# Kernel optimization log

Measured on AMD Instinct MI355X. Metric: run time of the kernel, lower is better.

The kernel has to match this reference:

```python
import jax, jax.numpy as jnp
import numpy as np

NUM_HEADS = 8
NUM_GROUPS = 32
EPS = 1e-5


def setup_inputs() -> dict:
    key = jax.random.key(0)
    ks = jax.random.split(key, 12)
    B, C, H, W = 8, 512, 32, 32
    E = 512
    s = 1.0 / np.sqrt(C)
    inp = {
        "input_tensor": jax.random.normal(ks[0], (B, C, H, W), dtype=jnp.float32),
        "Wq": jax.random.normal(ks[1], (C, E), dtype=jnp.float32) * s,
        "bq": jnp.zeros((E,), dtype=jnp.float32),
        "Wk": jax.random.normal(ks[2], (C, E), dtype=jnp.float32) * s,
        "bk": jnp.zeros((E,), dtype=jnp.float32),
        "Wv": jax.random.normal(ks[3], (C, E), dtype=jnp.float32) * s,
        "bv": jnp.zeros((E,), dtype=jnp.float32),
        "Wo": jax.random.normal(ks[4], (E, E), dtype=jnp.float32) * s,
        "bo": jnp.zeros((E,), dtype=jnp.float32),
        "gamma": jnp.ones((E,), dtype=jnp.float32),
        "beta": jnp.zeros((E,), dtype=jnp.float32),
    }
    return inp


def reference(input_tensor, Wq, bq, Wk, bk, Wv, bv, Wo, bo, gamma, beta):
    B, C, H, W = input_tensor.shape
    E = Wq.shape[1]
    nH = NUM_HEADS
    hd = E // nH
    S = H * W

    # [B, C, H, W] -> [B, S, C]
    x = input_tensor.reshape(B, C, S).transpose(0, 2, 1)

    q = (x @ Wq + bq).reshape(B, S, nH, hd).transpose(0, 2, 1, 3)  # [B, h, S, d]
    k = (x @ Wk + bk).reshape(B, S, nH, hd).transpose(0, 2, 1, 3)
    v = (x @ Wv + bv).reshape(B, S, nH, hd).transpose(0, 2, 1, 3)

    scale = hd ** (-0.5)
    scores = jnp.einsum("bhqd,bhkd->bhqk", q, k) * scale
    weights = jax.nn.softmax(scores, axis=-1)
    attn = jnp.einsum("bhqk,bhkd->bhqd", weights, v)  # [B, h, S, d]

    attn = attn.transpose(0, 2, 1, 3).reshape(B, S, E)
    out = attn @ Wo + bo  # [B, S, E]
    out = out.transpose(0, 2, 1).reshape(B, E, H, W)

    y = out + input_tensor

    # GroupNorm over (channels_per_group, H, W)
    G = NUM_GROUPS
    yg = y.reshape(B, G, E // G, H, W)
    mean = jnp.mean(yg, axis=(2, 3, 4), keepdims=True)
    var = jnp.var(yg, axis=(2, 3, 4), keepdims=True)
    yn = ((yg - mean) * jax.lax.rsqrt(var + EPS)).reshape(B, E, H, W)
    return yn * gamma[None, :, None, None] + beta[None, :, None, None]
```

## Files before the change

kernel.cpp:

```cpp
#include <hip/hip_runtime.h>
#include <math.h>

constexpr int Bn  = 8;
constexpr int Cc  = 512;
constexpr int Ss  = 1024;
constexpr int Ee  = 512;
constexpr int nHd = 8;
constexpr int Hd  = 64;
constexpr int Gg  = 32;
constexpr int Cpg = 16;

typedef __bf16 bf16x8 __attribute__((ext_vector_type(8)));
typedef float  f32x4  __attribute__((ext_vector_type(4)));
typedef float  f32x16 __attribute__((ext_vector_type(16)));

__device__ inline __bf16 cvt_bf16(float f) {
    unsigned u = __builtin_bit_cast(unsigned, f);
    u += 0x7fffu + ((u >> 16) & 1u);
    unsigned short h = (unsigned short)(u >> 16);
    return __builtin_bit_cast(__bf16, h);
}

__device__ inline void gld16(const __bf16* g, __bf16* l) {
    __builtin_amdgcn_global_load_lds(
        (const __attribute__((address_space(1))) void*)g,
        (__attribute__((address_space(3))) void*)l, 16, 0, 0);
}

__device__ inline unsigned pk_bf16_rtz(float hi, float lo) {
    return __builtin_amdgcn_perm(__builtin_bit_cast(unsigned, hi),
                                 __builtin_bit_cast(unsigned, lo), 0x07060302u);
}

__global__ __launch_bounds__(256) void transpose_x(
    const float* __restrict__ x, __bf16* __restrict__ xt)
{
    const int b = blockIdx.z, c0 = blockIdx.y * 32, s0 = blockIdx.x * 32;
    __shared__ float T[32][33];
    const int r8 = threadIdx.x >> 5, c32 = threadIdx.x & 31;
#pragma unroll
    for (int i = 0; i < 4; i++)
        T[r8 + i * 8][c32] = x[((size_t)b * Cc + c0 + r8 + i * 8) * Ss + s0 + c32];
    __syncthreads();
#pragma unroll
    for (int i = 0; i < 4; i++)
        xt[((size_t)b * Ss + s0 + r8 + i * 8) * Cc + c0 + c32] =
            cvt_bf16(T[c32][r8 + i * 8]);
}

__global__ __launch_bounds__(256) void transpose_w(
    const float* __restrict__ w0, const float* __restrict__ w1,
    const float* __restrict__ w2, const float* __restrict__ w3,
    __bf16* __restrict__ d0, __bf16* __restrict__ d1,
    __bf16* __restrict__ d2, __bf16* __restrict__ d3)
{
    const int m = blockIdx.z;
    const float* src = (m == 0) ? w0 : (m == 1) ? w1 : (m == 2) ? w2 : w3;
    __bf16* dst = (m == 0) ? d0 : (m == 1) ? d1 : (m == 2) ? d2 : d3;
    const int e0 = blockIdx.x * 32, c0 = blockIdx.y * 32;
    __shared__ float T[32][33];
    const int r8 = threadIdx.x >> 5, c32 = threadIdx.x & 31;
#pragma unroll
    for (int i = 0; i < 4; i++)
        T[r8 + i * 8][c32] = src[(size_t)(c0 + r8 + i * 8) * Ee + e0 + c32];
    __syncthreads();
#pragma unroll
    for (int i = 0; i < 4; i++)
        dst[(size_t)(e0 + r8 + i * 8) * Cc + c0 + c32] = cvt_bf16(T[c32][r8 + i * 8]);
}

__global__ __launch_bounds__(256) void qkv_mfma(
    const __bf16* __restrict__ xt,
    const __bf16* __restrict__ wqt, const __bf16* __restrict__ wkt,
    const __bf16* __restrict__ wvt,
    const float* __restrict__ bq, const float* __restrict__ bk,
    const float* __restrict__ bv,
    __bf16* __restrict__ qb, __bf16* __restrict__ kb, __bf16* __restrict__ vt)
{
    const int b = blockIdx.z;
    const int wsel = blockIdx.y >> 2;
    const int e0 = (blockIdx.y & 3) * 128;
    const int s0 = blockIdx.x * 128;
    const __bf16* A  = xt + (size_t)b * Ss * Cc;
    const __bf16* Bm = (wsel == 0) ? wqt : (wsel == 1) ? wkt : wvt;
    const float*  bias = (wsel == 0) ? bq : (wsel == 1) ? bk : bv;

    __shared__ __align__(16) __bf16 As[128 * 32];
    __shared__ __align__(16) __bf16 Bs[128 * 32];
    __shared__ __align__(16) __bf16 T[128 * 136];

    const int wave = threadIdx.x >> 6, lane = threadIdx.x & 63;
    const int lid = lane & 15, quad = lane >> 4;
    const int wm = wave & 1, wn = wave >> 1;
    const int srow = lane >> 2, sch = lane & 3;

    f32x4 acc[4][4] = {};

    for (int k0 = 0; k0 < Cc; k0 += 32) {
#pragma unroll
        for (int i = 0; i < 2; i++) {
            const int inst = wave * 2 + i;
            const int r = inst * 16 + srow;
            gld16(&A [(size_t)(s0 + r) * Cc + k0 + sch * 8], &As[inst * 512]);
            gld16(&Bm[(size_t)(e0 + r) * Cc + k0 + sch * 8], &Bs[inst * 512]);
        }
        __syncthreads();
        bf16x8 af[4], bf[4];
#pragma unroll
        for (int i = 0; i < 4; i++)
            af[i] = *(const bf16x8*)&As[(wm * 64 + i * 16 + lid) * 32 + quad * 8];
#pragma unroll
        for (int j = 0; j < 4; j++)
            bf[j] = *(const bf16x8*)&Bs[(wn * 64 + j * 16 + lid) * 32 + quad * 8];
#pragma unroll
        for (int i = 0; i < 4; i++)
#pragma unroll
            for (int j = 0; j < 4; j++)
                acc[i][j] = __builtin_amdgcn_mfma_f32_16x16x32_bf16(
                    af[i], bf[j], acc[i][j], 0, 0, 0);
        __syncthreads();
    }

    float bj[4];
#pragma unroll
    for (int j = 0; j < 4; j++) bj[j] = bias[e0 + wn * 64 + j * 16 + lid];

    if (wsel == 2) {
#pragma unroll
        for (int i = 0; i < 4; i++) {
            const int s4 = wm * 64 + i * 16 + quad * 4;
#pragma unroll
            for (int j = 0; j < 4; j++) {
                const int e_l = wn * 64 + j * 16 + lid;
                unsigned short u0 = __builtin_bit_cast(unsigned short, cvt_bf16(acc[i][j][0] + bj[j]));
                unsigned short u1 = __builtin_bit_cast(unsigned short, cvt_bf16(acc[i][j][1] + bj[j]));
                unsigned short u2 = __builtin_bit_cast(unsigned short, cvt_bf16(acc[i][j][2] + bj[j]));
                unsigned short u3 = __builtin_bit_cast(unsigned short, cvt_bf16(acc[i][j][3] + bj[j]));
                uint2 pk;
                pk.x = (unsigned)u0 | ((unsigned)u1 << 16);
                pk.y = (unsigned)u2 | ((unsigned)u3 << 16);
                *(uint2*)&T[e_l * 136 + s4] = pk;
            }
        }
        __syncthreads();
        const int t = threadIdx.x;
#pragma unroll
        for (int it = 0; it < 8; it++) {
            const int idx = t + it * 256;
            const int e_l = idx >> 4, c8 = (idx & 15) * 8;
            bf16x8 val = *(const bf16x8*)&T[e_l * 136 + c8];
            const int e_g = e0 + e_l;
            const int head = e_g >> 6, d = e_g & 63;
            *(bf16x8*)&vt[(((size_t)b * nHd + head) * Hd + d) * Ss + s0 + c8] = val;
        }
    } else {
        __bf16* outp = (wsel == 0) ? qb : kb;
#pragma unroll
        for (int i = 0; i < 4; i++) {
#pragma unroll
            for (int j = 0; j < 4; j++) {
                const int e1 = e0 + wn * 64 + j * 16 + lid;
                const int head = e1 >> 6, d = e1 & 63;
#pragma unroll
                for (int r = 0; r < 4; r++) {
                    const int s1 = s0 + wm * 64 + i * 16 + quad * 4 + r;
                    outp[(((size_t)b * nHd + head) * Ss + s1) * Hd + d] =
                        cvt_bf16(acc[i][j][r] + bj[j]);
                }
            }
        }
    }
}

__global__ __launch_bounds__(256, 2) void attn_mfma(
    const __bf16* __restrict__ q, const __bf16* __restrict__ k,
    const __bf16* __restrict__ vt, __bf16* __restrict__ attn_out)
{
    const int bh = blockIdx.x;
    const int s0 = blockIdx.y * 128;
    const __bf16* qp = q  + (size_t)bh * Ss * Hd;
    const __bf16* kp = k  + (size_t)bh * Ss * Hd;
    const __bf16* vp = vt + (size_t)bh * Hd * Ss;

    __shared__ __align__(16) __bf16 Ks[64 * 64];
    __shared__ __align__(16) __bf16 Vs[64 * 64];
    __shared__ __align__(16) __bf16 Ps[4][32 * 64];

    const int wave = threadIdx.x >> 6, lane = threadIdx.x & 63;
    const int nl = lane & 31, h = lane >> 5;
    __bf16* PsW = Ps[wave];

    const int sq = s0 + wave * 32 + nl;
    bf16x8 qf[4];
#pragma unroll
    for (int kk2 = 0; kk2 < 4; kk2++)
        qf[kk2] = *(const bf16x8*)&qp[(size_t)sq * Hd + kk2 * 16 + h * 8];

    f32x16 oacc[2] = {};
    float rs = 0.0f;
    const float cexp = 0.125f * 1.44269504f;

    const int srow = lane >> 3, sch = lane & 7;
    for (int kt = 0; kt < 16; kt++) {
#pragma unroll
        for (int i = 0; i < 2; i++) {
            const int inst = wave * 2 + i;
            const int rK = inst * 8 + srow;
            gld16(&kp[(size_t)(kt * 64 + rK) * Hd + ((sch ^ (rK & 7)) * 8)],
                  &Ks[inst * 512]);
            gld16(&vp[(size_t)rK * Ss + kt * 64 + ((sch ^ (rK & 7)) * 8)],
                  &Vs[inst * 512]);
        }
        __syncthreads();

        f32x16 sc[2] = {};
#pragma unroll
        for (int kk2 = 0; kk2 < 4; kk2++) {
#pragma unroll
            for (int mt = 0; mt < 2; mt++) {
                bf16x8 kf = *(const bf16x8*)&Ks[(mt * 32 + nl) * 64 +
                                                (((2 * kk2 + h) ^ (nl & 7)) * 8)];
                sc[mt] = __builtin_amdgcn_mfma_f32_32x32x16_bf16(
                    kf, qf[kk2], sc[mt], 0, 0, 0);
            }
        }

#pragma unroll
        for (int mt = 0; mt < 2; mt++) {
            float p[16];
#pragma unroll
            for (int r = 0; r < 16; r++) {
                p[r] = __builtin_amdgcn_exp2f(sc[mt][r] * cexp);
                rs += p[r];
            }
#pragma unroll
            for (int g = 0; g < 4; g++) {
                uint2 pk;
                pk.x = pk_bf16_rtz(p[4 * g + 1], p[4 * g + 0]);
                pk.y = pk_bf16_rtz(p[4 * g + 3], p[4 * g + 2]);
                const int ch = (2 * g + h + 8 * mt) ^ ((nl & 7) << 1);
                *(uint2*)&PsW[nl * 64 + ch * 4] = pk;
            }
        }

#pragma unroll
        for (int kk = 0; kk < 4; kk++) {
            const int cp = (4 * kk + 2 * h) ^ ((nl & 7) << 1);
            bf16x8 pf = *(const bf16x8*)&PsW[nl * 64 + cp * 4];
#pragma unroll
            for (int dt = 0; dt < 2; dt++) {
                bf16x8 vf = *(const bf16x8*)&Vs[(dt * 32 + nl) * 64 +
                                                (((2 * kk + h) ^ (nl & 7)) * 8)];
                oacc[dt] = __builtin_amdgcn_mfma_f32_32x32x16_bf16(
                    pf, vf, oacc[dt], 0, 0, 0);
            }
        }
        __syncthreads();
    }

    rs += __shfl_xor(rs, 32, 64);
    const float inv = 1.0f / rs;
    const int b = bh >> 3, head = bh & 7;
#pragma unroll
    for (int r = 0; r < 16; r++) {
        const int rowq = (r & 3) + 8 * (r >> 2) + 4 * h;
        const float invr = __shfl(inv, rowq, 64);
        const int s1 = s0 + wave * 32 + rowq;
#pragma unroll
        for (int dt = 0; dt < 2; dt++)
            attn_out[((size_t)b * Ss + s1) * Ee + head * Hd + dt * 32 + nl] =
                cvt_bf16(oacc[dt][r] * invr);
    }
}

__global__ __launch_bounds__(256) void outproj_mfma(
    const __bf16* __restrict__ attnb, const __bf16* __restrict__ wot,
    const float* __restrict__ bo, const float* __restrict__ xin,
    float* __restrict__ y)
{
    const int b  = blockIdx.z;
    const int e0 = blockIdx.y * 128;
    const int s0 = blockIdx.x * 128;
    const __bf16* Bm = attnb + (size_t)b * Ss * Ee;

    __shared__ __align__(16) __bf16 As[128 * 32];
    __shared__ __align__(16) __bf16 Bs[128 * 32];

    const int wave = threadIdx.x >> 6, lane = threadIdx.x & 63;
    const int lid = lane & 15, quad = lane >> 4;
    const int wm = wave & 1, wn = wave >> 1;
    const int srow = lane >> 2, sch = lane & 3;

    f32x4 acc[4][4] = {};

    for (int k0 = 0; k0 < Ee; k0 += 32) {
#pragma unroll
        for (int i = 0; i < 2; i++) {
            const int inst = wave * 2 + i;
            const int r = inst * 16 + srow;
            gld16(&wot[(size_t)(e0 + r) * Ee + k0 + sch * 8], &As[inst * 512]);
            gld16(&Bm [(size_t)(s0 + r) * Ee + k0 + sch * 8], &Bs[inst * 512]);
        }
        __syncthreads();
        bf16x8 af[4], bf[4];
#pragma unroll
        for (int i = 0; i < 4; i++)
            af[i] = *(const bf16x8*)&As[(wm * 64 + i * 16 + lid) * 32 + quad * 8];
#pragma unroll
        for (int j = 0; j < 4; j++)
            bf[j] = *(const bf16x8*)&Bs[(wn * 64 + j * 16 + lid) * 32 + quad * 8];
#pragma unroll
        for (int i = 0; i < 4; i++)
#pragma unroll
            for (int j = 0; j < 4; j++)
                acc[i][j] = __builtin_amdgcn_mfma_f32_16x16x32_bf16(
                    af[i], bf[j], acc[i][j], 0, 0, 0);
        __syncthreads();
    }

#pragma unroll
    for (int i = 0; i < 4; i++) {
#pragma unroll
        for (int r = 0; r < 4; r++) {
            const int eo1 = e0 + wm * 64 + i * 16 + quad * 4 + r;
            const float bb = bo[eo1];
#pragma unroll
            for (int j = 0; j < 4; j++) {
                const int s1 = s0 + wn * 64 + j * 16 + lid;
                const size_t idx = ((size_t)b * Ee + eo1) * Ss + s1;
                y[idx] = acc[i][j][r] + bb + xin[idx];
            }
        }
    }
}

__global__ __launch_bounds__(256) void gnorm_kernel(
    const float* __restrict__ y, const float* __restrict__ gamma,
    const float* __restrict__ beta, float* __restrict__ out)
{
    const int bg = blockIdx.x;
    const int b = bg >> 5, g = bg & 31;
    const size_t base = ((size_t)b * Ee + g * Cpg) * Ss;
    const float4* y4 = (const float4*)(y + base);
    constexpr int N4 = (Cpg * Ss) / 4;

    float s = 0.f, s2 = 0.f;
    for (int i = threadIdx.x; i < N4; i += 256) {
        float4 vv = y4[i];
        s  += vv.x + vv.y + vv.z + vv.w;
        s2 += vv.x * vv.x + vv.y * vv.y + vv.z * vv.z + vv.w * vv.w;
    }
#pragma unroll
    for (int off = 32; off > 0; off >>= 1) {
        s  += __shfl_down(s, off, 64);
        s2 += __shfl_down(s2, off, 64);
    }
    __shared__ float red[8];
    __shared__ float stats[2];
    const int lane = threadIdx.x & 63, wid = threadIdx.x >> 6;
    if (lane == 0) { red[wid] = s; red[4 + wid] = s2; }
    __syncthreads();
    if (threadIdx.x == 0) {
        float ts  = red[0] + red[1] + red[2] + red[3];
        float ts2 = red[4] + red[5] + red[6] + red[7];
        float mean = ts / (float)(Cpg * Ss);
        float var  = ts2 / (float)(Cpg * Ss) - mean * mean;
        stats[0] = mean;
        stats[1] = rsqrtf(var + 1e-5f);
    }
    __syncthreads();
    const float mean = stats[0], rstd = stats[1];
    float4* o4 = (float4*)(out + base);
    for (int i = threadIdx.x; i < N4; i += 256) {
        float4 vv = y4[i];
        const int c = g * Cpg + (i >> 8);
        const float gm = gamma[c] * rstd;
        const float bt = beta[c];
        float4 r;
        r.x = (vv.x - mean) * gm + bt;
        r.y = (vv.y - mean) * gm + bt;
        r.z = (vv.z - mean) * gm + bt;
        r.w = (vv.w - mean) * gm + bt;
        o4[i] = r;
    }
}

extern "C" void kernel_launch(void* const* d_in, const int* in_sizes, int n_in,
                              void* d_out, int out_size, void* d_ws, size_t ws_size,
                              hipStream_t stream)
{
    const float* x     = (const float*)d_in[0];
    const float* Wq    = (const float*)d_in[1];
    const float* bq    = (const float*)d_in[2];
    const float* Wk    = (const float*)d_in[3];
    const float* bk    = (const float*)d_in[4];
    const float* Wv    = (const float*)d_in[5];
    const float* bv    = (const float*)d_in[6];
    const float* Wo    = (const float*)d_in[7];
    const float* bo    = (const float*)d_in[8];
    const float* gamma = (const float*)d_in[9];
    const float* beta  = (const float*)d_in[10];
    float* out = (float*)d_out;

    char* ws = (char*)d_ws;
    __bf16* xt    = (__bf16*)ws;
    __bf16* wqt   = (__bf16*)(ws + (8u << 20));
    __bf16* wkt   = (__bf16*)(ws + (8u << 20) + (512u << 10));
    __bf16* wvt   = (__bf16*)(ws + (9u << 20));
    __bf16* wot   = (__bf16*)(ws + (9u << 20) + (512u << 10));
    __bf16* qb    = (__bf16*)(ws + (10u << 20));
    __bf16* kb    = (__bf16*)(ws + (18u << 20));
    __bf16* vtb   = (__bf16*)(ws + (26u << 20));
    __bf16* attnb = (__bf16*)(ws + (34u << 20));
    float*  yb    = (float*) (ws + (42u << 20));

    transpose_x<<<dim3(Ss / 32, Cc / 32, Bn), 256, 0, stream>>>(x, xt);
    transpose_w<<<dim3(Ee / 32, Cc / 32, 4), 256, 0, stream>>>(
        Wq, Wk, Wv, Wo, wqt, wkt, wvt, wot);

    qkv_mfma<<<dim3(Ss / 128, 12, Bn), 256, 0, stream>>>(
        xt, wqt, wkt, wvt, bq, bk, bv, qb, kb, vtb);

    attn_mfma<<<dim3(Bn * nHd, Ss / 128), 256, 0, stream>>>(qb, kb, vtb, attnb);

    outproj_mfma<<<dim3(Ss / 128, Ee / 128, Bn), 256, 0, stream>>>(
        attnb, wot, bo, x, yb);

    gnorm_kernel<<<Bn * Gg, 256, 0, stream>>>(yb, gamma, beta, out);
}
```

Measured before the change: 168.4 us.

## Merge transpose kernels, widen attention key tiles, alias qkv LDS, store residual sum in bf16

Merges the input and weight transposes into one launch, which removes a kernel launch. The attention kernel now processes 128 keys per iteration instead of 64 and uses a wider XOR swizzle, halving loop trips and barriers at the cost of more LDS. The qkv GEMM aliases its staging buffers with the output transpose buffer to cut LDS use. The pre-norm sum y is stored as bf16 instead of fp32, halving its write and two reads in groupnorm at some precision cost.

```diff
diff --git a/kernel.cpp b/kernel.cpp
--- a/kernel.cpp
+++ b/kernel.cpp
@@ -32,41 +32,42 @@
                                  __builtin_bit_cast(unsigned, lo), 0x07060302u);
 }
 
-__global__ __launch_bounds__(256) void transpose_x(
-    const float* __restrict__ x, __bf16* __restrict__ xt)
-{
-    const int b = blockIdx.z, c0 = blockIdx.y * 32, s0 = blockIdx.x * 32;
-    __shared__ float T[32][33];
-    const int r8 = threadIdx.x >> 5, c32 = threadIdx.x & 31;
-#pragma unroll
-    for (int i = 0; i < 4; i++)
-        T[r8 + i * 8][c32] = x[((size_t)b * Cc + c0 + r8 + i * 8) * Ss + s0 + c32];
-    __syncthreads();
-#pragma unroll
-    for (int i = 0; i < 4; i++)
-        xt[((size_t)b * Ss + s0 + r8 + i * 8) * Cc + c0 + c32] =
-            cvt_bf16(T[c32][r8 + i * 8]);
-}
-
-__global__ __launch_bounds__(256) void transpose_w(
+__global__ __launch_bounds__(256) void transpose_xw(
+    const float* __restrict__ x, __bf16* __restrict__ xt,
     const float* __restrict__ w0, const float* __restrict__ w1,
     const float* __restrict__ w2, const float* __restrict__ w3,
     __bf16* __restrict__ d0, __bf16* __restrict__ d1,
     __bf16* __restrict__ d2, __bf16* __restrict__ d3)
 {
-    const int m = blockIdx.z;
-    const float* src = (m == 0) ? w0 : (m == 1) ? w1 : (m == 2) ? w2 : w3;
-    __bf16* dst = (m == 0) ? d0 : (m == 1) ? d1 : (m == 2) ? d2 : d3;
-    const int e0 = blockIdx.x * 32, c0 = blockIdx.y * 32;
     __shared__ float T[32][33];
     const int r8 = threadIdx.x >> 5, c32 = threadIdx.x & 31;
-#pragma unroll
-    for (int i = 0; i < 4; i++)
-        T[r8 + i * 8][c32] = src[(size_t)(c0 + r8 + i * 8) * Ee + e0 + c32];
-    __syncthreads();
-#pragma unroll
-    for (int i = 0; i < 4; i++)
-        dst[(size_t)(e0 + r8 + i * 8) * Cc + c0 + c32] = cvt_bf16(T[c32][r8 + i * 8]);
+    const int z = blockIdx.z;
+    if (z < 8) {
+        const int b = z, c0 = blockIdx.y * 32, s0 = blockIdx.x * 32;
+#pragma unroll
+        for (int i = 0; i < 4; i++)
+            T[r8 + i * 8][c32] =
+                x[((size_t)b * Cc + c0 + r8 + i * 8) * Ss + s0 + c32];
+        __syncthreads();
+#pragma unroll
+        for (int i = 0; i < 4; i++)
+            xt[((size_t)b * Ss + s0 + r8 + i * 8) * Cc + c0 + c32] =
+                cvt_bf16(T[c32][r8 + i * 8]);
+    } else {
+        if (blockIdx.x >= 16) return;
+        const int m = z - 8;
+        const float* src = (m == 0) ? w0 : (m == 1) ? w1 : (m == 2) ? w2 : w3;
+        __bf16* dst = (m == 0) ? d0 : (m == 1) ? d1 : (m == 2) ? d2 : d3;
+        const int e0 = blockIdx.x * 32, c0 = blockIdx.y * 32;
+#pragma unroll
+        for (int i = 0; i < 4; i++)
+            T[r8 + i * 8][c32] = src[(size_t)(c0 + r8 + i * 8) * Ee + e0 + c32];
+        __syncthreads();
+#pragma unroll
+        for (int i = 0; i < 4; i++)
+            dst[(size_t)(e0 + r8 + i * 8) * Cc + c0 + c32] =
+                cvt_bf16(T[c32][r8 + i * 8]);
+    }
 }
 
 __global__ __launch_bounds__(256) void qkv_mfma(
@@ -85,9 +86,10 @@
     const __bf16* Bm = (wsel == 0) ? wqt : (wsel == 1) ? wkt : wvt;
     const float*  bias = (wsel == 0) ? bq : (wsel == 1) ? bk : bv;
 
-    __shared__ __align__(16) __bf16 As[128 * 32];
-    __shared__ __align__(16) __bf16 Bs[128 * 32];
-    __shared__ __align__(16) __bf16 T[128 * 136];
+    __shared__ __align__(16) char smem[128 * 136 * 2];
+    __bf16* As = (__bf16*)smem;
+    __bf16* Bs = (__bf16*)(smem + 8192);
+    __bf16* T  = (__bf16*)smem;
 
     const int wave = threadIdx.x >> 6, lane = threadIdx.x & 63;
     const int lid = lane & 15, quad = lane >> 4;
@@ -182,9 +184,9 @@
     const __bf16* kp = k  + (size_t)bh * Ss * Hd;
     const __bf16* vp = vt + (size_t)bh * Hd * Ss;
 
-    __shared__ __align__(16) __bf16 Ks[64 * 64];
-    __shared__ __align__(16) __bf16 Vs[64 * 64];
-    __shared__ __align__(16) __bf16 Ps[4][32 * 64];
+    __shared__ __align__(16) __bf16 Ks[128 * 64];
+    __shared__ __align__(16) __bf16 Vs[64 * 128];
+    __shared__ __align__(16) __bf16 Ps[4][32 * 128];
 
     const int wave = threadIdx.x >> 6, lane = threadIdx.x & 63;
     const int nl = lane & 31, h = lane >> 5;
@@ -200,24 +202,27 @@
     float rs = 0.0f;
     const float cexp = 0.125f * 1.44269504f;
 
-    const int srow = lane >> 3, sch = lane & 7;
-    for (int kt = 0; kt < 16; kt++) {
-#pragma unroll
-        for (int i = 0; i < 2; i++) {
-            const int inst = wave * 2 + i;
-            const int rK = inst * 8 + srow;
-            gld16(&kp[(size_t)(kt * 64 + rK) * Hd + ((sch ^ (rK & 7)) * 8)],
+    const int srow8 = lane >> 3, sch8 = lane & 7;
+    const int srow4 = lane >> 4, sch16 = lane & 15;
+
+    for (int kt = 0; kt < 8; kt++) {
+#pragma unroll
+        for (int i = 0; i < 4; i++) {
+            const int inst = wave * 4 + i;
+            const int rK = inst * 8 + srow8;
+            gld16(&kp[(size_t)(kt * 128 + rK) * Hd + ((sch8 ^ (rK & 7)) * 8)],
                   &Ks[inst * 512]);
-            gld16(&vp[(size_t)rK * Ss + kt * 64 + ((sch ^ (rK & 7)) * 8)],
+            const int dR = inst * 4 + srow4;
+            gld16(&vp[(size_t)dR * Ss + kt * 128 + ((sch16 ^ (dR & 15)) * 8)],
                   &Vs[inst * 512]);
         }
         __syncthreads();
 
-        f32x16 sc[2] = {};
+        f32x16 sc[4] = {};
 #pragma unroll
         for (int kk2 = 0; kk2 < 4; kk2++) {
 #pragma unroll
-            for (int mt = 0; mt < 2; mt++) {
+            for (int mt = 0; mt < 4; mt++) {
                 bf16x8 kf = *(const bf16x8*)&Ks[(mt * 32 + nl) * 64 +
                                                 (((2 * kk2 + h) ^ (nl & 7)) * 8)];
                 sc[mt] = __builtin_amdgcn_mfma_f32_32x32x16_bf16(
@@ -226,7 +231,7 @@
         }
 
 #pragma unroll
-        for (int mt = 0; mt < 2; mt++) {
+        for (int mt = 0; mt < 4; mt++) {
             float p[16];
 #pragma unroll
             for (int r = 0; r < 16; r++) {
@@ -238,19 +243,19 @@
                 uint2 pk;
                 pk.x = pk_bf16_rtz(p[4 * g + 1], p[4 * g + 0]);
                 pk.y = pk_bf16_rtz(p[4 * g + 3], p[4 * g + 2]);
-                const int ch = (2 * g + h + 8 * mt) ^ ((nl & 7) << 1);
-                *(uint2*)&PsW[nl * 64 + ch * 4] = pk;
-            }
-        }
-
-#pragma unroll
-        for (int kk = 0; kk < 4; kk++) {
-            const int cp = (4 * kk + 2 * h) ^ ((nl & 7) << 1);
-            bf16x8 pf = *(const bf16x8*)&PsW[nl * 64 + cp * 4];
+                const int gr = (mt * 8 + 2 * g + h) ^ ((nl & 15) << 1);
+                *(uint2*)&PsW[nl * 128 + gr * 4] = pk;
+            }
+        }
+
+#pragma unroll
+        for (int kk = 0; kk < 8; kk++) {
+            const int cp = (kk * 2 + h) ^ (nl & 15);
+            bf16x8 pf = *(const bf16x8*)&PsW[nl * 128 + cp * 8];
 #pragma unroll
             for (int dt = 0; dt < 2; dt++) {
-                bf16x8 vf = *(const bf16x8*)&Vs[(dt * 32 + nl) * 64 +
-                                                (((2 * kk + h) ^ (nl & 7)) * 8)];
+                bf16x8 vf = *(const bf16x8*)&Vs[(dt * 32 + nl) * 128 +
+                                                (((kk * 2 + h) ^ (nl & 15)) * 8)];
                 oacc[dt] = __builtin_amdgcn_mfma_f32_32x32x16_bf16(
                     pf, vf, oacc[dt], 0, 0, 0);
             }
@@ -276,7 +281,7 @@
 __global__ __launch_bounds__(256) void outproj_mfma(
     const __bf16* __restrict__ attnb, const __bf16* __restrict__ wot,
     const float* __restrict__ bo, const float* __restrict__ xin,
-    float* __restrict__ y)
+    __bf16* __restrict__ y)
 {
     const int b  = blockIdx.z;
     const int e0 = blockIdx.y * 128;
@@ -328,27 +333,30 @@
             for (int j = 0; j < 4; j++) {
                 const int s1 = s0 + wn * 64 + j * 16 + lid;
                 const size_t idx = ((size_t)b * Ee + eo1) * Ss + s1;
-                y[idx] = acc[i][j][r] + bb + xin[idx];
+                y[idx] = cvt_bf16(acc[i][j][r] + bb + xin[idx]);
             }
         }
     }
 }
 
 __global__ __launch_bounds__(256) void gnorm_kernel(
-    const float* __restrict__ y, const float* __restrict__ gamma,
+    const __bf16* __restrict__ y, const float* __restrict__ gamma,
     const float* __restrict__ beta, float* __restrict__ out)
 {
     const int bg = blockIdx.x;
     const int b = bg >> 5, g = bg & 31;
     const size_t base = ((size_t)b * Ee + g * Cpg) * Ss;
-    const float4* y4 = (const float4*)(y + base);
-    constexpr int N4 = (Cpg * Ss) / 4;
+    const bf16x8* y8 = (const bf16x8*)(y + base);
+    constexpr int N8 = (Cpg * Ss) / 8;
 
     float s = 0.f, s2 = 0.f;
-    for (int i = threadIdx.x; i < N4; i += 256) {
-        float4 vv = y4[i];
-        s  += vv.x + vv.y + vv.z + vv.w;
-        s2 += vv.x * vv.x + vv.y * vv.y + vv.z * vv.z + vv.w * vv.w;
+    for (int i = threadIdx.x; i < N8; i += 256) {
+        bf16x8 vv = y8[i];
+#pragma unroll
+        for (int j = 0; j < 8; j++) {
+            const float f = (float)vv[j];
+            s += f; s2 += f * f;
+        }
     }
 #pragma unroll
     for (int off = 32; off > 0; off >>= 1) {
@@ -370,18 +378,18 @@
     }
     __syncthreads();
     const float mean = stats[0], rstd = stats[1];
-    float4* o4 = (float4*)(out + base);
-    for (int i = threadIdx.x; i < N4; i += 256) {
-        float4 vv = y4[i];
-        const int c = g * Cpg + (i >> 8);
+    for (int i = threadIdx.x; i < N8; i += 256) {
+        bf16x8 vv = y8[i];
+        const int c = g * Cpg + (i >> 7);
         const float gm = gamma[c] * rstd;
         const float bt = beta[c];
-        float4 r;
-        r.x = (vv.x - mean) * gm + bt;
-        r.y = (vv.y - mean) * gm + bt;
-        r.z = (vv.z - mean) * gm + bt;
-        r.w = (vv.w - mean) * gm + bt;
-        o4[i] = r;
+        f32x4 r0, r1;
+#pragma unroll
+        for (int j = 0; j < 4; j++) r0[j] = ((float)vv[j] - mean) * gm + bt;
+#pragma unroll
+        for (int j = 0; j < 4; j++) r1[j] = ((float)vv[4 + j] - mean) * gm + bt;
+        *(f32x4*)&out[base + (size_t)i * 8]     = r0;
+        *(f32x4*)&out[base + (size_t)i * 8 + 4] = r1;
     }
 }
 
@@ -412,11 +420,10 @@
     __bf16* kb    = (__bf16*)(ws + (18u << 20));
     __bf16* vtb   = (__bf16*)(ws + (26u << 20));
     __bf16* attnb = (__bf16*)(ws + (34u << 20));
-    float*  yb    = (float*) (ws + (42u << 20));
-
-    transpose_x<<<dim3(Ss / 32, Cc / 32, Bn), 256, 0, stream>>>(x, xt);
-    transpose_w<<<dim3(Ee / 32, Cc / 32, 4), 256, 0, stream>>>(
-        Wq, Wk, Wv, Wo, wqt, wkt, wvt, wot);
+    __bf16* yb    = (__bf16*)(ws + (42u << 20));
+
+    transpose_xw<<<dim3(32, 16, 12), 256, 0, stream>>>(
+        x, xt, Wq, Wk, Wv, Wo, wqt, wkt, wvt, wot);
 
     qkv_mfma<<<dim3(Ss / 128, 12, Bn), 256, 0, stream>>>(
         xt, wqt, wkt, wvt, bq, bk, bv, qb, kb, vtb);
```

Result: faster. 161.4 us (-4.1%).
